# Optimization experiments

Measured on AMD Instinct MI355X. Metric: run time of the kernel, lower is better.

## Reference

```python
import jax, jax.numpy as jnp
import numpy as np

EPS = 1e-5
HEADS = 4
C = 128
GROUPS = 32  # min(32, 128//4)
SR = 2
SCALE = (C // HEADS) ** -0.5


def group_norm(x, gamma, beta, groups=GROUPS, eps=EPS):
    N, Ch, H, W = x.shape
    xg = x.reshape(N, groups, Ch // groups, H, W)
    mu = xg.mean(axis=(2, 3, 4), keepdims=True)
    var = xg.var(axis=(2, 3, 4), keepdims=True)
    xg = (xg - mu) * jax.lax.rsqrt(var + eps)
    x = xg.reshape(N, Ch, H, W)
    return x * gamma[None, :, None, None] + beta[None, :, None, None]


def conv1x1(x, W, b):
    # x: [N,C,H,W], W: [Cout,Cin], b: [Cout]
    return jnp.einsum('nchw,oc->nohw', x, W) + b[None, :, None, None]


def avg_pool2(x):
    N, Ch, H, W = x.shape
    return x.reshape(N, Ch, H // SR, SR, W // SR, SR).mean(axis=(3, 5))


def to_heads(x):
    # [N,C,H,W] -> [N,h,HW,C//h]  (matches view(N,h,C/h,HW).permute(0,1,3,2))
    N, Ch, H, W = x.shape
    return x.reshape(N, HEADS, Ch // HEADS, H * W).transpose(0, 1, 3, 2)


def setup_inputs() -> dict:
    key = jax.random.key(0)
    ks = jax.random.split(key, 16)
    B, H, W = 8, 64, 64
    s = 1.0 / np.sqrt(C)
    inp = {
        'q_src': jax.random.normal(ks[0], (B, C, H, W), jnp.float32),
        'k_src': jax.random.normal(ks[1], (B, C, H, W), jnp.float32),
        'v_src': jax.random.normal(ks[2], (B, C, H, W), jnp.float32),
        'Wq': jax.random.normal(ks[3], (C, C), jnp.float32) * s,
        'bq': jnp.zeros((C,), jnp.float32),
        'Wk': jax.random.normal(ks[4], (C, C), jnp.float32) * s,
        'bk': jnp.zeros((C,), jnp.float32),
        'Wv': jax.random.normal(ks[5], (C, C), jnp.float32) * s,
        'bv': jnp.zeros((C,), jnp.float32),
        'Wp': jax.random.normal(ks[6], (C, C), jnp.float32) * s,
        'bp': jnp.zeros((C,), jnp.float32),
        'g_nq': jnp.ones((C,), jnp.float32), 'b_nq': jnp.zeros((C,), jnp.float32),
        'g_nk': jnp.ones((C,), jnp.float32), 'b_nk': jnp.zeros((C,), jnp.float32),
        'g_nv': jnp.ones((C,), jnp.float32), 'b_nv': jnp.zeros((C,), jnp.float32),
        'g_srk': jnp.ones((C,), jnp.float32), 'b_srk': jnp.zeros((C,), jnp.float32),
        'g_srv': jnp.ones((C,), jnp.float32), 'b_srv': jnp.zeros((C,), jnp.float32),
    }
    return inp


def reference(q_src, k_src, v_src, Wq, bq, Wk, bk, Wv, bv, Wp, bp,
              g_nq, b_nq, g_nk, b_nk, g_nv, b_nv, g_srk, b_srk, g_srv, b_srv):
    # Q path: GN -> 1x1 conv
    q = conv1x1(group_norm(q_src, g_nq, b_nq), Wq, bq)
    # K/V paths: SR (avgpool + GN) -> GN -> 1x1 conv
    k = conv1x1(group_norm(group_norm(avg_pool2(k_src), g_srk, b_srk), g_nk, b_nk), Wk, bk)
    v = conv1x1(group_norm(group_norm(avg_pool2(v_src), g_srv, b_srv), g_nv, b_nv), Wv, bv)

    N, Cq, Hq, Wq_ = q.shape
    qh, kh, vh = to_heads(q), to_heads(k), to_heads(v)  # [N,h,L,d]
    attn = jnp.einsum('nhqd,nhkd->nhqk', qh * SCALE, kh)  # [N,h,Lq,Lk]
    attn = jax.nn.softmax(attn, axis=-1)
    out = jnp.einsum('nhqk,nhkd->nhqd', attn, vh)  # [N,h,Lq,d]
    out = out.transpose(0, 1, 3, 2).reshape(N, Cq, Hq, Wq_)
    return conv1x1(out, Wp, bp)
```

## Files before the change

### kernel.cpp

```cpp
#include <hip/hip_runtime.h>

typedef __attribute__((ext_vector_type(8)))  short s8v;
typedef __attribute__((ext_vector_type(4)))  short s4v;
typedef __attribute__((ext_vector_type(16))) float f16v;
typedef __attribute__((ext_vector_type(2)))  int   i2v;
typedef __attribute__((ext_vector_type(2)))  float f2v;

__device__ __forceinline__ unsigned short f2bf(float f) {
  union { float f; unsigned u; } v; v.f = f;
  unsigned r = v.u + 0x7FFFu + ((v.u >> 16) & 1u);
  return (unsigned short)(r >> 16);
}
__device__ __forceinline__ float bf2f(unsigned short b) {
  return __uint_as_float((unsigned)b << 16);
}
__device__ __forceinline__ float fexp2(float x) {
#if __has_builtin(__builtin_amdgcn_exp2f)
  return __builtin_amdgcn_exp2f(x);
#else
  return exp2f(x);
#endif
}
__device__ __forceinline__ f2v mk2(float a, float b) { f2v r; r[0] = a; r[1] = b; return r; }

__device__ __forceinline__ void gn_stats_body(
    int blk, const float* __restrict__ x, const float* __restrict__ gamma,
    const float* __restrict__ beta, float* __restrict__ ab, float* sh)
{
  int n = blk >> 5, g = blk & 31;
  int t = threadIdx.x; int cl = t >> 6, lane = t & 63;
  const float4* x4 = (const float4*)(x + (size_t)(n * 128 + g * 4 + cl) * 4096);
  float s = 0.f, ss = 0.f;
  #pragma unroll
  for (int j = 0; j < 16; ++j) {
    float4 v = x4[lane + 64 * j];
    s  += v.x + v.y + v.z + v.w;
    ss += v.x * v.x + v.y * v.y + v.z * v.z + v.w * v.w;
  }
  #pragma unroll
  for (int m = 32; m >= 1; m >>= 1) { s += __shfl_xor(s, m); ss += __shfl_xor(ss, m); }
  if (lane == 0) { sh[cl] = s; sh[4 + cl] = ss; }
  __syncthreads();
  if (t < 4) {
    float mu = (sh[0] + sh[1] + sh[2] + sh[3]) * (1.f / 16384.f);
    float e  = (sh[4] + sh[5] + sh[6] + sh[7]) * (1.f / 16384.f);
    float r  = rsqrtf(e - mu * mu + 1e-5f);
    int c = g * 4 + t;
    float al = gamma[c] * r;
    ab[n * 128 + c] = al;
    ab[1024 + n * 128 + c] = beta[c] - mu * al;
  }
}

__device__ __forceinline__ void pool_aff_body(
    int blk, const float* __restrict__ x,
    const float* __restrict__ g1, const float* __restrict__ b1,
    const float* __restrict__ g2, const float* __restrict__ b2,
    float* __restrict__ pooled, float* __restrict__ ab, float* sh)
{
  int n = blk >> 5, g = blk & 31;
  int t = threadIdx.x; int cl = t >> 6, lane = t & 63;
  int c = g * 4 + cl;
  const float* xb = x + (size_t)(n * 128 + c) * 4096;
  float* pb = pooled + (size_t)(n * 128 + c) * 1024;
  float s = 0.f, ss = 0.f;
  #pragma unroll
  for (int j = 0; j < 16; ++j) {
    int p = lane + 64 * j;
    int py = p >> 5, px = p & 31;
    float2 a = ((const float2*)(xb + py * 128))[px];
    float2 b = ((const float2*)(xb + py * 128 + 64))[px];
    float v = 0.25f * (a.x + a.y + b.x + b.y);
    pb[p] = v; s += v; ss += v * v;
  }
  #pragma unroll
  for (int m = 32; m >= 1; m >>= 1) { s += __shfl_xor(s, m); ss += __shfl_xor(ss, m); }
  if (lane == 0) { sh[cl] = s; sh[4 + cl] = ss; }
  __syncthreads();
  if (t < 4) {
    float mu1 = (sh[0] + sh[1] + sh[2] + sh[3]) * (1.f / 4096.f);
    float e1  = (sh[4] + sh[5] + sh[6] + sh[7]) * (1.f / 4096.f);
    float r1  = rsqrtf(e1 - mu1 * mu1 + 1e-5f);
    float mzs = 0.f, e2s = 0.f;
    #pragma unroll
    for (int cc = 0; cc < 4; ++cc) {
      int ch = g * 4 + cc;
      float a = r1 * g1[ch];
      float d = b1[ch] - mu1 * a;
      float m = sh[cc] * (1.f / 1024.f);
      float q = sh[4 + cc] * (1.f / 1024.f);
      mzs += a * m + d;
      e2s += a * a * q + 2.f * a * d * m + d * d;
    }
    float mu2 = 0.25f * mzs;
    float r2  = rsqrtf(0.25f * e2s - mu2 * mu2 + 1e-5f);
    int ch = g * 4 + t;
    float a = r1 * g1[ch];
    float d = b1[ch] - mu1 * a;
    ab[n * 128 + ch] = a * r2 * g2[ch];
    ab[1024 + n * 128 + ch] = (d - mu2) * r2 * g2[ch] + b2[ch];
  }
}

__device__ __forceinline__ void wsplit_body(
    int b, const float* __restrict__ W, unsigned short* __restrict__ whi,
    unsigned short* __restrict__ wlo)
{
  int idx = b * 256 + threadIdx.x;
  #pragma unroll
  for (int k = 0; k < 4; ++k) {
    int f = idx + k * 4096;
    int o = f >> 7, c = f & 127;
    float v = W[f];
    unsigned short hb = f2bf(v);
    unsigned short lb = f2bf(v - bf2f(hb));
    int cq = c >> 2;
    int adr = (o * 16 + ((cq >> 1) ^ (o & 7))) * 8 + (cq & 1) * 4 + (c & 3);
    whi[adr] = hb; wlo[adr] = lb;
  }
}

__global__ __launch_bounds__(256) void prep_k(
    const float* __restrict__ q_src, const float* __restrict__ g_nq, const float* __restrict__ b_nq,
    const float* __restrict__ k_src, const float* __restrict__ g_srk, const float* __restrict__ b_srk,
    const float* __restrict__ g_nk, const float* __restrict__ b_nk,
    const float* __restrict__ v_src, const float* __restrict__ g_srv, const float* __restrict__ b_srv,
    const float* __restrict__ g_nv, const float* __restrict__ b_nv,
    const float* __restrict__ Wp,
    float* __restrict__ qab, float* __restrict__ kab, float* __restrict__ vab,
    float* __restrict__ knp, float* __restrict__ vnp,
    unsigned short* __restrict__ whi, unsigned short* __restrict__ wlo)
{
  __shared__ float sh[8];
  int b = blockIdx.x;
  if (b < 256) gn_stats_body(b, q_src, g_nq, b_nq, qab, sh);
  else if (b < 512) pool_aff_body(b - 256, k_src, g_srk, b_srk, g_nk, b_nk, knp, kab, sh);
  else if (b < 768) pool_aff_body(b - 512, v_src, g_srv, b_srv, g_nv, b_nv, vnp, vab, sh);
  else wsplit_body(b - 768, Wp, whi, wlo);
}

__device__ __forceinline__ void conv_body(
    int blk, const float* __restrict__ x, const float* __restrict__ ab,
    const float* __restrict__ W, const float* __restrict__ bias,
    unsigned short* __restrict__ po, int S, float outScale, int vt_mode,
    unsigned short* smem)
{
  unsigned short* Wsw = smem;
  unsigned short* xsw = smem + 16384;
  int t = threadIdx.x;
  int spb = S >> 7;
  int n  = blk / spb;
  int s0 = (blk % spb) << 7;

  #pragma unroll
  for (int k = 0; k < 16; ++k) {
    int f4 = t + (k << 8);
    int o = f4 >> 5, cq = f4 & 31;
    float4 wq = *(const float4*)(W + (size_t)o * 128 + cq * 4);
    s4v hv;
    hv[0] = (short)f2bf(wq.x); hv[1] = (short)f2bf(wq.y);
    hv[2] = (short)f2bf(wq.z); hv[3] = (short)f2bf(wq.w);
    *(s4v*)(Wsw + (o * 16 + ((cq >> 1) ^ (o & 7))) * 8 + (cq & 1) * 4) = hv;
  }
  int sl = t & 127, coh = t >> 7;
  for (int co = coh; co < 16; co += 2) {
    const float* xb = x + (size_t)(n * 128 + co * 8) * S + s0 + sl;
    const float* aa = ab + n * 128 + co * 8;
    const float* bb = aa + 1024;
    union { unsigned short u[8]; s8v v; } xv;
    #pragma unroll
    for (int e = 0; e < 8; ++e) xv.u[e] = f2bf(fmaf(xb[(size_t)e * S], aa[e], bb[e]));
    *(s8v*)(xsw + (co * 128 + sl) * 8) = xv.v;
  }
  __syncthreads();

  int lane = t & 63, w = t >> 6;
  int l31 = lane & 31, h = lane >> 5;
  int wo = (w & 1) << 6, wsp = (w >> 1) << 6;
  f16v acc00 = {}, acc01 = {}, acc10 = {}, acc11 = {};
  #pragma unroll
  for (int reg = 0; reg < 16; ++reg) {
    int rm = (reg & 3) + ((reg >> 2) << 3) + (h << 2);
    float b0 = bias[wo + rm], b1 = bias[wo + 32 + rm];
    acc00[reg] = b0; acc01[reg] = b0; acc10[reg] = b1; acc11[reg] = b1;
  }
  const s8v* Wv = (const s8v*)Wsw;
  const s8v* Xv = (const s8v*)xsw;
  int o0 = wo + l31, o1 = wo + 32 + l31;
  #pragma unroll
  for (int cs = 0; cs < 8; ++cs) {
    int kk = cs * 2 + h;
    s8v a0 = Wv[o0 * 16 + (kk ^ (o0 & 7))];
    s8v a1 = Wv[o1 * 16 + (kk ^ (o1 & 7))];
    s8v b0 = Xv[kk * 128 + wsp + l31];
    s8v b1 = Xv[kk * 128 + wsp + 32 + l31];
    acc00 = __builtin_amdgcn_mfma_f32_32x32x16_bf16(a0, b0, acc00, 0, 0, 0);
    acc01 = __builtin_amdgcn_mfma_f32_32x32x16_bf16(a0, b1, acc01, 0, 0, 0);
    acc10 = __builtin_amdgcn_mfma_f32_32x32x16_bf16(a1, b0, acc10, 0, 0, 0);
    acc11 = __builtin_amdgcn_mfma_f32_32x32x16_bf16(a1, b1, acc11, 0, 0, 0);
  }
  __syncthreads();
  unsigned short* ot = smem;
  #pragma unroll
  for (int reg = 0; reg < 16; ++reg) {
    int rm = (reg & 3) + ((reg >> 2) << 3) + (h << 2);
    ot[(wo + rm) * 132 + wsp + l31]           = f2bf(acc00[reg] * outScale);
    ot[(wo + rm) * 132 + wsp + 32 + l31]      = f2bf(acc01[reg] * outScale);
    ot[(wo + 32 + rm) * 132 + wsp + l31]      = f2bf(acc10[reg] * outScale);
    ot[(wo + 32 + rm) * 132 + wsp + 32 + l31] = f2bf(acc11[reg] * outScale);
  }
  __syncthreads();
  if (!vt_mode) {
    int d = t & 31;
    for (int i = 0; i < 64; ++i) {
      int idx2 = (t >> 5) + (i << 3);
      int s = idx2 & 127, ohi_ = idx2 >> 7;
      po[((size_t)(n * 4 + ohi_) * S + s0 + s) * 32 + d] = ot[(ohi_ * 32 + d) * 132 + s];
    }
  } else {
    int s = t & 127;
    for (int i = 0; i < 64; ++i) {
      int rr = (t >> 7) + i * 2;
      po[((size_t)(n * 4 + (rr >> 5)) * 32 + (rr & 31)) * S + s0 + s] = ot[rr * 132 + s];
    }
  }
}

__global__ __launch_bounds__(256) void convs_k(
    const float* __restrict__ q_src, const float* __restrict__ qab,
    const float* __restrict__ Wq, const float* __restrict__ bq, unsigned short* __restrict__ qhb,
    const float* __restrict__ knp, const float* __restrict__ kab,
    const float* __restrict__ Wk, const float* __restrict__ bk, unsigned short* __restrict__ khb,
    const float* __restrict__ vnp, const float* __restrict__ vab,
    const float* __restrict__ Wv, const float* __restrict__ bv, unsigned short* __restrict__ vtb,
    float qscale)
{
  __shared__ __align__(16) unsigned short smem[32768];
  int b = blockIdx.x;
  if (b < 256)      conv_body(b,       q_src, qab, Wq, bq, qhb, 4096, qscale, 0, smem);
  else if (b < 320) conv_body(b - 256, knp,   kab, Wk, bk, khb, 1024, 1.0f,   0, smem);
  else              conv_body(b - 320, vnp,   vab, Wv, bv, vtb, 1024, 1.0f,   1, smem);
}

__global__ __launch_bounds__(256) void conv_hilo_k(
    const unsigned short* __restrict__ xhi, const unsigned short* __restrict__ xlo,
    const unsigned short* __restrict__ whi, const unsigned short* __restrict__ wlo,
    const float* __restrict__ bias, float* __restrict__ out, int S)
{
  __shared__ __align__(16) unsigned short smem[32768];
  unsigned short* Whi = smem;
  unsigned short* Wlo = smem + 8192;
  unsigned short* Xhi = smem + 16384;
  unsigned short* Xlo = smem + 24576;
  int t = threadIdx.x;
  int spb = S >> 6;
  int bid = blockIdx.x;
  int oh_ = bid & 1;
  int sb  = (bid >> 1) % spb;
  int n   = (bid >> 1) / spb;
  int s0  = sb << 6;

  #pragma unroll
  for (int i = 0; i < 4; ++i) {
    int u = t + i * 256;
    ((s8v*)Whi)[u] = ((const s8v*)(whi + oh_ * 8192))[u];
    ((s8v*)Wlo)[u] = ((const s8v*)(wlo + oh_ * 8192))[u];
  }
  #pragma unroll
  for (int i = 0; i < 4; ++i) {
    int co = t & 15, slx = (t >> 4) + i * 16;
    size_t g = ((size_t)n * 4096 + s0 + slx) * 128 + co * 8;
    int dst = ((co * 64 + slx) * 8) ^ ((co & 7) << 3);
    *(s8v*)(Xhi + dst) = *(const s8v*)(xhi + g);
    *(s8v*)(Xlo + dst) = *(const s8v*)(xlo + g);
  }
  __syncthreads();

  int lane = t & 63, w = t >> 6;
  int l31 = lane & 31, h = lane >> 5;
  int ol  = ((w & 1) << 5) + l31;
  int s_l = ((w >> 1) << 5) + l31;
  f16v acc = {};
  #pragma unroll
  for (int reg = 0; reg < 16; ++reg) {
    int rm = (reg & 3) + ((reg >> 2) << 3) + (h << 2);
    acc[reg] = bias[oh_ * 64 + ((w & 1) << 5) + rm];
  }
  const s8v* WHv = (const s8v*)Whi;
  const s8v* WLv = (const s8v*)Wlo;
  #pragma unroll
  for (int cs = 0; cs < 8; ++cs) {
    int kk = cs * 2 + h;
    int ia = ol * 16 + (kk ^ (ol & 7));
    int ix = ((kk * 64 + s_l) * 8) ^ ((kk & 7) << 3);
    s8v ah = WHv[ia], al = WLv[ia];
    s8v bh = *(const s8v*)(Xhi + ix);
    s8v bl = *(const s8v*)(Xlo + ix);
    acc = __builtin_amdgcn_mfma_f32_32x32x16_bf16(ah, bh, acc, 0, 0, 0);
    acc = __builtin_amdgcn_mfma_f32_32x32x16_bf16(ah, bl, acc, 0, 0, 0);
    acc = __builtin_amdgcn_mfma_f32_32x32x16_bf16(al, bh, acc, 0, 0, 0);
  }
  #pragma unroll
  for (int reg = 0; reg < 16; ++reg) {
    int rm = (reg & 3) + ((reg >> 2) << 3) + (h << 2);
    out[(size_t)(n * 128 + oh_ * 64 + ((w & 1) << 5) + rm) * S + s0 + s_l] = acc[reg];
  }
}

__global__ __launch_bounds__(256, 4) void attn_k(
    const unsigned short* __restrict__ qh, const unsigned short* __restrict__ kh,
    const unsigned short* __restrict__ vt, unsigned short* __restrict__ ohi,
    unsigned short* __restrict__ olo)
{
  __shared__ __align__(16) unsigned short Klds[2][2048];
  __shared__ __align__(16) unsigned short Vlds[2][2048];
  __shared__ float linv[128];
  int t = threadIdx.x;
  int lane = t & 63, w = t >> 6;
  int l31 = lane & 31, h = lane >> 5;
  int blk = blockIdx.x;
  int nh = blk & 31, qb = blk >> 5;

  const unsigned short* qp = qh + (((size_t)nh * 4096 + qb * 128 + w * 32 + l31) << 5);
  s8v qf0 = *(const s8v*)(qp + h * 8);
  s8v qf1 = *(const s8v*)(qp + (2 + h) * 8);

  size_t kvb = (size_t)nh << 15;
  const unsigned short* kg = kh + kvb + ((t >> 2) << 5) + ((t & 3) << 3);
  const unsigned short* vg = vt + kvb + ((size_t)(t >> 3) << 10) + ((t & 7) << 3);
  int ku = ((t >> 2) << 2) + ((t & 3) ^ ((t >> 3) & 3));
  int vu = ((t >> 3) << 3) + ((t & 7) ^ ((t >> 3) & 7));

  s8v rk = *(const s8v*)kg;
  s8v rv = *(const s8v*)vg;
  *(s8v*)&Klds[0][ku * 8] = rk;
  *(s8v*)&Vlds[0][vu * 8] = rv;

  const f16v fz = {};
  f16v oacc = fz;
  f2v lp0 = mk2(0.f, 0.f), lp1 = mk2(0.f, 0.f);
  int kx = (l31 >> 1) & 3;
  int vx = l31 & 7;

  #pragma unroll 2
  for (int tile = 0; tile < 16; ++tile) {
    int buf = tile & 1;
    __syncthreads();
    if (tile < 15) {
      int j0 = (tile + 1) << 6;
      rk = *(const s8v*)(kg + (size_t)j0 * 32);
      rv = *(const s8v*)(vg + j0);
    }
    const unsigned short* Kb = Klds[buf];
    const unsigned short* Vb = Vlds[buf];
    #pragma unroll
    for (int s = 0; s < 2; ++s) {
      int rb = s * 128 + l31 * 4;
      s8v kf0 = *(const s8v*)(Kb + ((rb + (h ^ kx)) << 3));
      s8v kf1 = *(const s8v*)(Kb + ((rb + ((2 + h) ^ kx)) << 3));
      f16v sf = __builtin_amdgcn_mfma_f32_32x32x16_bf16(kf0, qf0, fz, 0, 0, 0);
      sf = __builtin_amdgcn_mfma_f32_32x32x16_bf16(kf1, qf1, sf, 0, 0, 0);
      float p[16];
      #pragma unroll
      for (int r = 0; r < 16; ++r) p[r] = fexp2(sf[r]);
      lp0 += mk2(p[0], p[1]);  lp1 += mk2(p[2], p[3]);
      lp0 += mk2(p[4], p[5]);  lp1 += mk2(p[6], p[7]);
      lp0 += mk2(p[8], p[9]);  lp1 += mk2(p[10], p[11]);
      lp0 += mk2(p[12], p[13]); lp1 += mk2(p[14], p[15]);
      unsigned c[8];
      #pragma unroll
      for (int q = 0; q < 8; ++q)
        asm("v_cvt_pk_bf16_f32 %0, %1, %2" : "=v"(c[q]) : "v"(p[2 * q]), "v"(p[2 * q + 1]));
      i2v s02 = __builtin_amdgcn_permlane32_swap((int)c[0], (int)c[2], false, false);
      i2v s13 = __builtin_amdgcn_permlane32_swap((int)c[1], (int)c[3], false, false);
      i2v s46 = __builtin_amdgcn_permlane32_swap((int)c[4], (int)c[6], false, false);
      i2v s57 = __builtin_amdgcn_permlane32_swap((int)c[5], (int)c[7], false, false);
      union { int u[4]; s8v v; } u0, u1;
      u0.u[0] = s02[0]; u0.u[1] = s13[0]; u0.u[2] = s02[1]; u0.u[3] = s13[1];
      u1.u[0] = s46[0]; u1.u[1] = s57[0]; u1.u[2] = s46[1]; u1.u[3] = s57[1];
      s8v vf0 = *(const s8v*)(Vb + ((l31 * 8 + ((s * 4 + h) ^ vx)) << 3));
      s8v vf1 = *(const s8v*)(Vb + ((l31 * 8 + ((s * 4 + 2 + h) ^ vx)) << 3));
      oacc = __builtin_amdgcn_mfma_f32_32x32x16_bf16(u0.v, vf0, oacc, 0, 0, 0);
      oacc = __builtin_amdgcn_mfma_f32_32x32x16_bf16(u1.v, vf1, oacc, 0, 0, 0);
    }
    if (tile < 15) {
      *(s8v*)&Klds[buf ^ 1][ku * 8] = rk;
      *(s8v*)&Vlds[buf ^ 1][vu * 8] = rv;
    }
  }

  float l_part = lp0[0] + lp0[1] + lp1[0] + lp1[1];
  float l_tot = l_part + __shfl_xor(l_part, 32);
  if (h == 0) linv[w * 32 + l31] = 1.0f / l_tot;
  __syncthreads();
  int n = nh >> 2, hh = nh & 3;
  size_t obase = ((size_t)n * 4096 + qb * 128) * 128 + hh * 32 + l31;
  #pragma unroll
  for (int reg = 0; reg < 16; ++reg) {
    int rm = (reg & 3) + ((reg >> 2) << 3) + (h << 2);
    float val = oacc[reg] * linv[w * 32 + rm];
    unsigned short hb = f2bf(val);
    unsigned short lb = f2bf(val - bf2f(hb));
    size_t adr = obase + (size_t)(w * 32 + rm) * 128;
    ohi[adr] = hb; olo[adr] = lb;
  }
}

extern "C" void kernel_launch(void* const* d_in, const int* in_sizes, int n_in,
                              void* d_out, int out_size, void* d_ws, size_t ws_size,
                              hipStream_t stream)
{
  (void)in_sizes; (void)n_in; (void)out_size; (void)ws_size;
  const float* q_src = (const float*)d_in[0];
  const float* k_src = (const float*)d_in[1];
  const float* v_src = (const float*)d_in[2];
  const float* Wq = (const float*)d_in[3];
  const float* bq = (const float*)d_in[4];
  const float* Wk = (const float*)d_in[5];
  const float* bk = (const float*)d_in[6];
  const float* Wv = (const float*)d_in[7];
  const float* bv = (const float*)d_in[8];
  const float* Wp = (const float*)d_in[9];
  const float* bp = (const float*)d_in[10];
  const float* g_nq  = (const float*)d_in[11];
  const float* b_nq  = (const float*)d_in[12];
  const float* g_nk  = (const float*)d_in[13];
  const float* b_nk  = (const float*)d_in[14];
  const float* g_nv  = (const float*)d_in[15];
  const float* b_nv  = (const float*)d_in[16];
  const float* g_srk = (const float*)d_in[17];
  const float* b_srk = (const float*)d_in[18];
  const float* g_srv = (const float*)d_in[19];
  const float* b_srv = (const float*)d_in[20];

  unsigned short* qhb = (unsigned short*)d_ws;
  unsigned short* khb = qhb + 4194304;
  unsigned short* vtb = khb + 1048576;
  unsigned short* ohi = vtb + 1048576;
  unsigned short* olo = ohi + 4194304;
  float* knp = (float*)(olo + 4194304);
  float* vnp = knp + 1048576;
  float* qab = vnp + 1048576;
  float* kab = qab + 2048;
  float* vab = kab + 2048;
  unsigned short* whi = (unsigned short*)(vab + 2048);
  unsigned short* wlo = whi + 16384;

  const float QSCALE = 0.17677669529663688f * 1.44269504088896340f;

  prep_k<<<784, 256, 0, stream>>>(q_src, g_nq, b_nq,
                                  k_src, g_srk, b_srk, g_nk, b_nk,
                                  v_src, g_srv, b_srv, g_nv, b_nv,
                                  Wp, qab, kab, vab, knp, vnp, whi, wlo);
  convs_k<<<384, 256, 0, stream>>>(q_src, qab, Wq, bq, qhb,
                                   knp, kab, Wk, bk, khb,
                                   vnp, vab, Wv, bv, vtb, QSCALE);
  attn_k<<<1024, 256, 0, stream>>>(qhb, khb, vtb, ohi, olo);
  conv_hilo_k<<<1024, 256, 0, stream>>>(ohi, olo, whi, wlo, bp, (float*)d_out, 4096);
}
```

Baseline: 70.68 us.

## Pass fp32 attention output, split hi/lo in projection, vectorize pooling, setprio MFMAs

The attention kernel now writes fp32 output once, and the projection kernel does the bf16 hi/lo split itself. The projection kernel is also restructured into 32-position tiles with all 128 output channels per block, and its weights are loaded straight into registers instead of going through LDS. Other changes: pooling loads are widened to float4, bf16 conversions use the packed v_cvt_pk_bf16_f32 instruction, and s_setprio is placed around the MFMAs in attention. Several unrelated micro-optimizations are bundled together, and the packed convert may round differently from the earlier software rounding.

```diff
diff --git a/kernel.cpp b/kernel.cpp
--- a/kernel.cpp
+++ b/kernel.cpp
@@ -65,13 +65,17 @@
   float* pb = pooled + (size_t)(n * 128 + c) * 1024;
   float s = 0.f, ss = 0.f;
   #pragma unroll
-  for (int j = 0; j < 16; ++j) {
-    int p = lane + 64 * j;
-    int py = p >> 5, px = p & 31;
-    float2 a = ((const float2*)(xb + py * 128))[px];
-    float2 b = ((const float2*)(xb + py * 128 + 64))[px];
-    float v = 0.25f * (a.x + a.y + b.x + b.y);
-    pb[p] = v; s += v; ss += v * v;
+  for (int j = 0; j < 8; ++j) {
+    int pp = (lane + 64 * j) * 2;
+    int py = pp >> 5, px2 = pp & 31;
+    const float* r0 = xb + py * 128 + px2 * 2;
+    float4 A = *(const float4*)r0;
+    float4 B = *(const float4*)(r0 + 64);
+    float v0 = 0.25f * (A.x + A.y + B.x + B.y);
+    float v1 = 0.25f * (A.z + A.w + B.z + B.w);
+    float2 wv; wv.x = v0; wv.y = v1;
+    *(float2*)(pb + pp) = wv;
+    s += v0 + v1; ss += v0 * v0 + v1 * v1;
   }
   #pragma unroll
   for (int m = 32; m >= 1; m >>= 1) { s += __shfl_xor(s, m); ss += __shfl_xor(ss, m); }
@@ -157,19 +161,23 @@
     int f4 = t + (k << 8);
     int o = f4 >> 5, cq = f4 & 31;
     float4 wq = *(const float4*)(W + (size_t)o * 128 + cq * 4);
-    s4v hv;
-    hv[0] = (short)f2bf(wq.x); hv[1] = (short)f2bf(wq.y);
-    hv[2] = (short)f2bf(wq.z); hv[3] = (short)f2bf(wq.w);
-    *(s4v*)(Wsw + (o * 16 + ((cq >> 1) ^ (o & 7))) * 8 + (cq & 1) * 4) = hv;
+    union { unsigned q[2]; s4v v; } hv;
+    asm("v_cvt_pk_bf16_f32 %0, %1, %2" : "=v"(hv.q[0]) : "v"(wq.x), "v"(wq.y));
+    asm("v_cvt_pk_bf16_f32 %0, %1, %2" : "=v"(hv.q[1]) : "v"(wq.z), "v"(wq.w));
+    *(s4v*)(Wsw + (o * 16 + ((cq >> 1) ^ (o & 7))) * 8 + (cq & 1) * 4) = hv.v;
   }
   int sl = t & 127, coh = t >> 7;
   for (int co = coh; co < 16; co += 2) {
     const float* xb = x + (size_t)(n * 128 + co * 8) * S + s0 + sl;
     const float* aa = ab + n * 128 + co * 8;
     const float* bb = aa + 1024;
-    union { unsigned short u[8]; s8v v; } xv;
+    float f[8];
     #pragma unroll
-    for (int e = 0; e < 8; ++e) xv.u[e] = f2bf(fmaf(xb[(size_t)e * S], aa[e], bb[e]));
+    for (int e = 0; e < 8; ++e) f[e] = fmaf(xb[(size_t)e * S], aa[e], bb[e]);
+    union { unsigned q[4]; s8v v; } xv;
+    #pragma unroll
+    for (int e = 0; e < 4; ++e)
+      asm("v_cvt_pk_bf16_f32 %0, %1, %2" : "=v"(xv.q[e]) : "v"(f[2*e]), "v"(f[2*e+1]));
     *(s8v*)(xsw + (co * 128 + sl) * 8) = xv.v;
   }
   __syncthreads();
@@ -243,74 +251,78 @@
 }
 
 __global__ __launch_bounds__(256) void conv_hilo_k(
-    const unsigned short* __restrict__ xhi, const unsigned short* __restrict__ xlo,
-    const unsigned short* __restrict__ whi, const unsigned short* __restrict__ wlo,
-    const float* __restrict__ bias, float* __restrict__ out, int S)
-{
-  __shared__ __align__(16) unsigned short smem[32768];
-  unsigned short* Whi = smem;
-  unsigned short* Wlo = smem + 8192;
-  unsigned short* Xhi = smem + 16384;
-  unsigned short* Xlo = smem + 24576;
+    const float* __restrict__ xo, const unsigned short* __restrict__ whi,
+    const unsigned short* __restrict__ wlo, const float* __restrict__ bias,
+    float* __restrict__ out)
+{
+  __shared__ __align__(16) unsigned short Xh[4096], Xl[4096];
   int t = threadIdx.x;
-  int spb = S >> 6;
-  int bid = blockIdx.x;
-  int oh_ = bid & 1;
-  int sb  = (bid >> 1) % spb;
-  int n   = (bid >> 1) / spb;
-  int s0  = sb << 6;
-
-  #pragma unroll
-  for (int i = 0; i < 4; ++i) {
-    int u = t + i * 256;
-    ((s8v*)Whi)[u] = ((const s8v*)(whi + oh_ * 8192))[u];
-    ((s8v*)Wlo)[u] = ((const s8v*)(wlo + oh_ * 8192))[u];
-  }
-  #pragma unroll
-  for (int i = 0; i < 4; ++i) {
-    int co = t & 15, slx = (t >> 4) + i * 16;
-    size_t g = ((size_t)n * 4096 + s0 + slx) * 128 + co * 8;
-    int dst = ((co * 64 + slx) * 8) ^ ((co & 7) << 3);
-    *(s8v*)(Xhi + dst) = *(const s8v*)(xhi + g);
-    *(s8v*)(Xlo + dst) = *(const s8v*)(xlo + g);
-  }
-  __syncthreads();
-
   int lane = t & 63, w = t >> 6;
   int l31 = lane & 31, h = lane >> 5;
-  int ol  = ((w & 1) << 5) + l31;
-  int s_l = ((w >> 1) << 5) + l31;
-  f16v acc = {};
-  #pragma unroll
-  for (int reg = 0; reg < 16; ++reg) {
-    int rm = (reg & 3) + ((reg >> 2) << 3) + (h << 2);
-    acc[reg] = bias[oh_ * 64 + ((w & 1) << 5) + rm];
-  }
-  const s8v* WHv = (const s8v*)Whi;
-  const s8v* WLv = (const s8v*)Wlo;
+  int n = blockIdx.x >> 7, s0 = (blockIdx.x & 127) << 5;
+
+  int ol = w * 32 + l31;
+  const s8v* WH = (const s8v*)whi;
+  const s8v* WL = (const s8v*)wlo;
+  s8v ah[8], al[8];
   #pragma unroll
   for (int cs = 0; cs < 8; ++cs) {
     int kk = cs * 2 + h;
     int ia = ol * 16 + (kk ^ (ol & 7));
-    int ix = ((kk * 64 + s_l) * 8) ^ ((kk & 7) << 3);
-    s8v ah = WHv[ia], al = WLv[ia];
-    s8v bh = *(const s8v*)(Xhi + ix);
-    s8v bl = *(const s8v*)(Xlo + ix);
-    acc = __builtin_amdgcn_mfma_f32_32x32x16_bf16(ah, bh, acc, 0, 0, 0);
-    acc = __builtin_amdgcn_mfma_f32_32x32x16_bf16(ah, bl, acc, 0, 0, 0);
-    acc = __builtin_amdgcn_mfma_f32_32x32x16_bf16(al, bh, acc, 0, 0, 0);
-  }
+    ah[cs] = WH[ia];
+    al[cs] = WL[ia];
+  }
+
+  #pragma unroll
+  for (int i = 0; i < 2; ++i) {
+    int co = t & 15, sl = (t >> 4) + i * 16;
+    const float* xp = xo + (((size_t)(n * 4096 + s0 + sl)) << 7) + co * 8;
+    float4 A = *(const float4*)xp;
+    float4 B = *(const float4*)(xp + 4);
+    float f[8] = {A.x, A.y, A.z, A.w, B.x, B.y, B.z, B.w};
+    union { unsigned q[4]; s8v v; } H, L;
+    #pragma unroll
+    for (int e = 0; e < 4; ++e) {
+      unsigned hp;
+      asm("v_cvt_pk_bf16_f32 %0, %1, %2" : "=v"(hp) : "v"(f[2*e]), "v"(f[2*e+1]));
+      H.q[e] = hp;
+      float h0 = __uint_as_float(hp << 16);
+      float h1 = __uint_as_float(hp & 0xFFFF0000u);
+      float l0 = f[2*e] - h0, l1 = f[2*e+1] - h1;
+      asm("v_cvt_pk_bf16_f32 %0, %1, %2" : "=v"(L.q[e]) : "v"(l0), "v"(l1));
+    }
+    int dst = ((co * 32 + sl) * 8) ^ ((co & 7) << 3);
+    *(s8v*)(Xh + dst) = H.v;
+    *(s8v*)(Xl + dst) = L.v;
+  }
+  __syncthreads();
+
+  f16v acc;
   #pragma unroll
   for (int reg = 0; reg < 16; ++reg) {
     int rm = (reg & 3) + ((reg >> 2) << 3) + (h << 2);
-    out[(size_t)(n * 128 + oh_ * 64 + ((w & 1) << 5) + rm) * S + s0 + s_l] = acc[reg];
+    acc[reg] = bias[w * 32 + rm];
+  }
+  #pragma unroll
+  for (int cs = 0; cs < 8; ++cs) {
+    int kk = cs * 2 + h;
+    int ix = ((kk * 32 + l31) * 8) ^ ((kk & 7) << 3);
+    s8v bh = *(const s8v*)(Xh + ix);
+    s8v bl = *(const s8v*)(Xl + ix);
+    acc = __builtin_amdgcn_mfma_f32_32x32x16_bf16(ah[cs], bh, acc, 0, 0, 0);
+    acc = __builtin_amdgcn_mfma_f32_32x32x16_bf16(ah[cs], bl, acc, 0, 0, 0);
+    acc = __builtin_amdgcn_mfma_f32_32x32x16_bf16(al[cs], bh, acc, 0, 0, 0);
+  }
+  #pragma unroll
+  for (int reg = 0; reg < 16; ++reg) {
+    int rm = (reg & 3) + ((reg >> 2) << 3) + (h << 2);
+    out[(size_t)(n * 128 + w * 32 + rm) * 4096 + s0 + l31] = acc[reg];
   }
 }
 
 __global__ __launch_bounds__(256, 4) void attn_k(
     const unsigned short* __restrict__ qh, const unsigned short* __restrict__ kh,
-    const unsigned short* __restrict__ vt, unsigned short* __restrict__ ohi,
-    unsigned short* __restrict__ olo)
+    const unsigned short* __restrict__ vt, float* __restrict__ obuf)
 {
   __shared__ __align__(16) unsigned short Klds[2][2048];
   __shared__ __align__(16) unsigned short Vlds[2][2048];
@@ -358,8 +370,10 @@
       int rb = s * 128 + l31 * 4;
       s8v kf0 = *(const s8v*)(Kb + ((rb + (h ^ kx)) << 3));
       s8v kf1 = *(const s8v*)(Kb + ((rb + ((2 + h) ^ kx)) << 3));
+      __builtin_amdgcn_s_setprio(1);
       f16v sf = __builtin_amdgcn_mfma_f32_32x32x16_bf16(kf0, qf0, fz, 0, 0, 0);
       sf = __builtin_amdgcn_mfma_f32_32x32x16_bf16(kf1, qf1, sf, 0, 0, 0);
+      __builtin_amdgcn_s_setprio(0);
       float p[16];
       #pragma unroll
       for (int r = 0; r < 16; ++r) p[r] = fexp2(sf[r]);
@@ -380,8 +394,10 @@
       u1.u[0] = s46[0]; u1.u[1] = s57[0]; u1.u[2] = s46[1]; u1.u[3] = s57[1];
       s8v vf0 = *(const s8v*)(Vb + ((l31 * 8 + ((s * 4 + h) ^ vx)) << 3));
       s8v vf1 = *(const s8v*)(Vb + ((l31 * 8 + ((s * 4 + 2 + h) ^ vx)) << 3));
+      __builtin_amdgcn_s_setprio(1);
       oacc = __builtin_amdgcn_mfma_f32_32x32x16_bf16(u0.v, vf0, oacc, 0, 0, 0);
       oacc = __builtin_amdgcn_mfma_f32_32x32x16_bf16(u1.v, vf1, oacc, 0, 0, 0);
+      __builtin_amdgcn_s_setprio(0);
     }
     if (tile < 15) {
       *(s8v*)&Klds[buf ^ 1][ku * 8] = rk;
@@ -394,15 +410,11 @@
   if (h == 0) linv[w * 32 + l31] = 1.0f / l_tot;
   __syncthreads();
   int n = nh >> 2, hh = nh & 3;
-  size_t obase = ((size_t)n * 4096 + qb * 128) * 128 + hh * 32 + l31;
+  size_t obase = (((size_t)n * 4096 + qb * 128) << 7) + hh * 32 + l31;
   #pragma unroll
   for (int reg = 0; reg < 16; ++reg) {
     int rm = (reg & 3) + ((reg >> 2) << 3) + (h << 2);
-    float val = oacc[reg] * linv[w * 32 + rm];
-    unsigned short hb = f2bf(val);
-    unsigned short lb = f2bf(val - bf2f(hb));
-    size_t adr = obase + (size_t)(w * 32 + rm) * 128;
-    ohi[adr] = hb; olo[adr] = lb;
+    obuf[obase + ((size_t)(w * 32 + rm) << 7)] = oacc[reg] * linv[w * 32 + rm];
   }
 }
 
@@ -436,13 +448,12 @@
   unsigned short* qhb = (unsigned short*)d_ws;
   unsigned short* khb = qhb + 4194304;
   unsigned short* vtb = khb + 1048576;
-  unsigned short* ohi = vtb + 1048576;
-  unsigned short* olo = ohi + 4194304;
-  float* knp = (float*)(olo + 4194304);
-  float* vnp = knp + 1048576;
-  float* qab = vnp + 1048576;
-  float* kab = qab + 2048;
-  float* vab = kab + 2048;
+  float* obuf = (float*)(vtb + 1048576);
+  float* knp  = obuf + 4194304;
+  float* vnp  = knp + 1048576;
+  float* qab  = vnp + 1048576;
+  float* kab  = qab + 2048;
+  float* vab  = kab + 2048;
   unsigned short* whi = (unsigned short*)(vab + 2048);
   unsigned short* wlo = whi + 16384;
 
@@ -455,6 +466,6 @@
   convs_k<<<384, 256, 0, stream>>>(q_src, qab, Wq, bq, qhb,
                                    knp, kab, Wk, bk, khb,
                                    vnp, vab, Wv, bv, vtb, QSCALE);
-  attn_k<<<1024, 256, 0, stream>>>(qhb, khb, vtb, ohi, olo);
-  conv_hilo_k<<<1024, 256, 0, stream>>>(ohi, olo, whi, wlo, bp, (float*)d_out, 4096);
-}
+  attn_k<<<1024, 256, 0, stream>>>(qhb, khb, vtb, obuf);
+  conv_hilo_k<<<1024, 256, 0, stream>>>(obuf, whi, wlo, bp, (float*)d_out);
+}
```

After: 70.42 us. Within noise of the previous version (-0.4%).
